# Kernel optimization log

Measured on AMD Instinct MI355X. Metric: run time of the kernel, lower is better.

## Reference

```python
import jax, jax.numpy as jnp
import numpy as np

N_NODES = 50000
N_EDGES = 800000
IN_DIM = 512
HEADS = 4
OUT_DIM = 64


def setup_inputs() -> dict:
    key = jax.random.key(0)
    k1, k2, k3, k4 = jax.random.split(key, 4)
    x = jax.random.normal(k1, (N_NODES, IN_DIM), dtype=jnp.float32)
    edges = jax.random.randint(k2, (N_EDGES, 2), 0, N_NODES, dtype=jnp.int32)
    W = jax.random.normal(k3, (IN_DIM, HEADS * OUT_DIM), dtype=jnp.float32) * 0.05
    a = jax.random.normal(k4, (HEADS, 2 * OUT_DIM), dtype=jnp.float32) * 0.05
    bias = jnp.zeros((HEADS * OUT_DIM,), dtype=jnp.float32)
    return {"x": x, "edges": edges, "W": W, "a": a, "bias": bias}


def reference(x, edges, W, a, bias):
    num_nodes = x.shape[0]
    # project: [N, H, D]
    h = (x @ W).reshape(num_nodes, HEADS, OUT_DIM)
    src = edges[:, 0]
    dst = edges[:, 1]
    # raw attention per edge, per head: e = sum(a * concat(h_src, h_dst))
    a_src = a[:, :OUT_DIM]   # [H, D]
    a_dst = a[:, OUT_DIM:]   # [H, D]
    # precompute per-node dot-products, then gather (avoids [E,H,2D] concat)
    s_src = jnp.einsum('nhd,hd->nh', h, a_src)  # [N, H]
    s_dst = jnp.einsum('nhd,hd->nh', h, a_dst)  # [N, H]
    e = s_src[src] + s_dst[dst]                 # [E, H]
    e = jax.nn.leaky_relu(e, negative_slope=0.2)
    # softmax over edges grouped by SOURCE node (as in original code)
    max_e = jax.ops.segment_max(e, src, num_segments=num_nodes)  # [N, H]
    exp_e = jnp.exp(e - max_e[src])
    sum_exp = jax.ops.segment_sum(exp_e, src, num_segments=num_nodes)
    alpha = exp_e / (sum_exp[src] + 1e-10)       # [E, H]
    # messages aggregated at DESTINATION node
    messages = alpha[:, :, None] * h[src]        # [E, H, D]
    out = jax.ops.segment_sum(messages, dst, num_segments=num_nodes)  # [N, H, D]
    out = out.reshape(num_nodes, HEADS * OUT_DIM) + bias
    return out
```

## Files before the change

### kernel.cpp

```cpp
#include <hip/hip_runtime.h>
#include <math.h>

#define IN_DIM 512
#define NH 4
#define OD 64
#define HD 256

typedef float  floatx4 __attribute__((ext_vector_type(4)));
typedef short  shortx8 __attribute__((ext_vector_type(8)));

__device__ __forceinline__ unsigned short f2bf(float x) {
    unsigned int u = __float_as_uint(x);
    u += 0x7fffu + ((u >> 16) & 1u);
    return (unsigned short)(u >> 16);
}
__device__ __forceinline__ float bf2f(unsigned short u) {
    return __uint_as_float(((unsigned int)u) << 16);
}

__global__ void init_kernel(int* __restrict__ heads, int M2) {
    int i = blockIdx.x * blockDim.x + threadIdx.x;
    if (i < M2) heads[i] = -1;
}

__global__ void convert_w_kernel(const float* __restrict__ W, ushort* __restrict__ Wt) {
    int t = blockIdx.x * blockDim.x + threadIdx.x;
    if (t >= 256 * 64) return;
    int n = t >> 6;
    int k8 = (t & 63) * 8;
    shortx8 v;
    #pragma unroll
    for (int j = 0; j < 8; ++j) v[j] = (short)f2bf(W[(size_t)(k8 + j) * HD + n]);
    *(shortx8*)&Wt[(size_t)n * IN_DIM + k8] = v;
}

__global__ __launch_bounds__(256) void gemm_kernel(const float* __restrict__ x,
                                                   const ushort* __restrict__ Wt,
                                                   ushort* __restrict__ h, int M) {
    __shared__ ushort As[64 * 64];
    __shared__ ushort Bs[256 * 64];
    const int tid = threadIdx.x;
    const int lane = tid & 63;
    const int w = tid >> 6;
    const int bm = blockIdx.x * 64;
    const int wn = w * 64;
    const int lm = lane & 15;
    const int lq = lane >> 4;
    floatx4 acc[4][4];
    #pragma unroll
    for (int i = 0; i < 4; ++i)
        #pragma unroll
        for (int j = 0; j < 4; ++j) acc[i][j] = (floatx4){0.f, 0.f, 0.f, 0.f};

    for (int k0 = 0; k0 < IN_DIM; k0 += 64) {
        #pragma unroll
        for (int j = 0; j < 2; ++j) {
            int ch = tid * 2 + j;
            int row = ch >> 3;
            int c = (ch & 7) ^ (row & 7);
            int gr = bm + row;
            shortx8 v = (shortx8){0, 0, 0, 0, 0, 0, 0, 0};
            if (gr < M) {
                const float* gp = &x[(size_t)gr * IN_DIM + k0 + c * 8];
                float4 v0 = *(const float4*)gp;
                float4 v1 = *(const float4*)(gp + 4);
                v[0] = (short)f2bf(v0.x); v[1] = (short)f2bf(v0.y);
                v[2] = (short)f2bf(v0.z); v[3] = (short)f2bf(v0.w);
                v[4] = (short)f2bf(v1.x); v[5] = (short)f2bf(v1.y);
                v[6] = (short)f2bf(v1.z); v[7] = (short)f2bf(v1.w);
            }
            *(shortx8*)&As[ch * 8] = v;
        }
        #pragma unroll
        for (int j = 0; j < 8; ++j) {
            int ch = j * 256 + tid;
            int row = ch >> 3;
            int c = (ch & 7) ^ (row & 7);
            const ushort* gp = &Wt[(size_t)row * IN_DIM + k0 + c * 8];
            __builtin_amdgcn_global_load_lds(
                (const __attribute__((address_space(1))) void*)gp,
                (__attribute__((address_space(3))) void*)&Bs[(size_t)(j * 256 + wn) * 8],
                16, 0, 0);
        }
        __syncthreads();
        #pragma unroll
        for (int kk = 0; kk < 2; ++kk) {
            shortx8 af[4], bfr[4];
            #pragma unroll
            for (int mt = 0; mt < 4; ++mt) {
                int row = mt * 16 + lm;
                int c = (kk * 4 + lq) ^ (row & 7);
                af[mt] = *(const shortx8*)&As[row * 64 + c * 8];
            }
            #pragma unroll
            for (int nt = 0; nt < 4; ++nt) {
                int row = wn + nt * 16 + lm;
                int c = (kk * 4 + lq) ^ (row & 7);
                bfr[nt] = *(const shortx8*)&Bs[row * 64 + c * 8];
            }
            #pragma unroll
            for (int mt = 0; mt < 4; ++mt)
                #pragma unroll
                for (int nt = 0; nt < 4; ++nt)
                    acc[mt][nt] = __builtin_amdgcn_mfma_f32_16x16x32_bf16(
                        af[mt], bfr[nt], acc[mt][nt], 0, 0, 0);
        }
        __syncthreads();
    }
    #pragma unroll
    for (int mt = 0; mt < 4; ++mt)
        #pragma unroll
        for (int r = 0; r < 4; ++r) {
            int m = bm + mt * 16 + lq * 4 + r;
            if (m < M) {
                #pragma unroll
                for (int nt = 0; nt < 4; ++nt)
                    h[(size_t)m * HD + wn + nt * 16 + lm] = f2bf(acc[mt][nt][r]);
            }
        }
}

__global__ void s_kernel(const ushort* __restrict__ h, const float* __restrict__ a,
                         float* __restrict__ s_src, float* __restrict__ s_dst, int M) {
    int lane = threadIdx.x & 63;
    int n = blockIdx.x * 4 + (threadIdx.x >> 6);
    if (n >= M) return;
    int head = lane >> 4;
    int d0 = (lane & 15) << 2;
    ushort4 hu = *(const ushort4*)&h[(size_t)n * HD + lane * 4];
    float h0 = bf2f(hu.x), h1 = bf2f(hu.y), h2 = bf2f(hu.z), h3 = bf2f(hu.w);
    float4 as = *(const float4*)&a[head * 2 * OD + d0];
    float4 ad = *(const float4*)&a[head * 2 * OD + OD + d0];
    float ps = h0 * as.x + h1 * as.y + h2 * as.z + h3 * as.w;
    float pd = h0 * ad.x + h1 * ad.y + h2 * ad.z + h3 * ad.w;
    #pragma unroll
    for (int off = 1; off < 16; off <<= 1) {
        ps += __shfl_xor(ps, off, 64);
        pd += __shfl_xor(pd, off, 64);
    }
    if ((lane & 15) == 0) {
        s_src[n * NH + head] = ps;
        s_dst[n * NH + head] = pd;
    }
}

__global__ void link_kernel(const int2* __restrict__ edges,
                            int* __restrict__ head_src, int* __restrict__ next_src,
                            int* __restrict__ head_dst, int* __restrict__ next_dst,
                            int E) {
    int i = blockIdx.x * blockDim.x + threadIdx.x;
    if (i >= E) return;
    int2 e = edges[i];
    next_src[i] = atomicExch(&head_src[e.x], i);
    next_dst[i] = atomicExch(&head_dst[e.y], i);
}

__global__ void src_sum_kernel(const int2* __restrict__ edges,
                               const int* __restrict__ head_src,
                               const int* __restrict__ next_src,
                               const float* __restrict__ s_src,
                               const float* __restrict__ s_dst,
                               float* __restrict__ inv_sum, int M) {
    int n = blockIdx.x * blockDim.x + threadIdx.x;
    if (n >= M) return;
    float4 ss = *(const float4*)&s_src[n * NH];
    float4 sum = make_float4(0.f, 0.f, 0.f, 0.f);
    for (int e = head_src[n]; e != -1;) {
        int nxt = next_src[e];
        int dst = edges[e].y;
        float4 sd = *(const float4*)&s_dst[dst * NH];
        float e0 = ss.x + sd.x, e1 = ss.y + sd.y, e2 = ss.z + sd.z, e3 = ss.w + sd.w;
        e0 = e0 > 0.f ? e0 : 0.2f * e0;
        e1 = e1 > 0.f ? e1 : 0.2f * e1;
        e2 = e2 > 0.f ? e2 : 0.2f * e2;
        e3 = e3 > 0.f ? e3 : 0.2f * e3;
        sum.x += __expf(e0); sum.y += __expf(e1);
        sum.z += __expf(e2); sum.w += __expf(e3);
        e = nxt;
    }
    float4 iv;
    iv.x = 1.f / (sum.x + 1e-10f); iv.y = 1.f / (sum.y + 1e-10f);
    iv.z = 1.f / (sum.z + 1e-10f); iv.w = 1.f / (sum.w + 1e-10f);
    *(float4*)&inv_sum[n * NH] = iv;
}

__global__ void gather_kernel(const int2* __restrict__ edges,
                              const int* __restrict__ head_dst,
                              const int* __restrict__ next_dst,
                              const float* __restrict__ s_src,
                              const float* __restrict__ s_dst,
                              const float* __restrict__ inv_sum,
                              const ushort* __restrict__ h,
                              const float* __restrict__ bias,
                              float* __restrict__ out, int M) {
    int lane = threadIdx.x & 63;
    int n = blockIdx.x * 4 + (threadIdx.x >> 6);
    if (n >= M) return;
    int head = lane >> 4;
    float sdst = s_dst[n * NH + head];
    float4 acc = *(const float4*)&bias[lane * 4];
    for (int e = head_dst[n]; e != -1;) {
        int nxt = next_dst[e];
        int src = edges[e].x;
        float es = s_src[src * NH + head] + sdst;
        es = es > 0.f ? es : 0.2f * es;
        float al = __expf(es) * inv_sum[src * NH + head];
        ushort4 hu = *(const ushort4*)&h[(size_t)src * HD + lane * 4];
        acc.x += al * bf2f(hu.x); acc.y += al * bf2f(hu.y);
        acc.z += al * bf2f(hu.z); acc.w += al * bf2f(hu.w);
        e = nxt;
    }
    *(float4*)&out[(size_t)n * HD + lane * 4] = acc;
}

extern "C" void kernel_launch(void* const* d_in, const int* in_sizes, int n_in,
                              void* d_out, int out_size, void* d_ws, size_t ws_size,
                              hipStream_t stream) {
    const float* x     = (const float*)d_in[0];
    const int2*  edges = (const int2*)d_in[1];
    const float* W     = (const float*)d_in[2];
    const float* a     = (const float*)d_in[3];
    const float* bias  = (const float*)d_in[4];
    float* out = (float*)d_out;
    const int M = in_sizes[0] / IN_DIM;
    const int E = in_sizes[1] / 2;

    char* p = (char*)d_ws;
    ushort* hB       = (ushort*)p; p += (size_t)M * HD * sizeof(ushort);
    ushort* Wt       = (ushort*)p; p += (size_t)HD * IN_DIM * sizeof(ushort);
    float*  s_src    = (float*)p;  p += (size_t)M * NH * sizeof(float);
    float*  s_dst    = (float*)p;  p += (size_t)M * NH * sizeof(float);
    float*  inv_sum  = (float*)p;  p += (size_t)M * NH * sizeof(float);
    int*    head_src = (int*)p;    p += (size_t)M * sizeof(int);
    int*    head_dst = (int*)p;    p += (size_t)M * sizeof(int);
    int*    next_src = (int*)p;    p += (size_t)E * sizeof(int);
    int*    next_dst = (int*)p;    p += (size_t)E * sizeof(int);

    init_kernel<<<(2 * M + 255) / 256, 256, 0, stream>>>(head_src, 2 * M);
    convert_w_kernel<<<64, 256, 0, stream>>>(W, Wt);
    gemm_kernel<<<(M + 63) / 64, 256, 0, stream>>>(x, Wt, hB, M);
    s_kernel<<<(M + 3) / 4, 256, 0, stream>>>(hB, a, s_src, s_dst, M);
    link_kernel<<<(E + 255) / 256, 256, 0, stream>>>(edges, head_src, next_src,
                                                     head_dst, next_dst, E);
    src_sum_kernel<<<(M + 255) / 256, 256, 0, stream>>>(edges, head_src, next_src,
                                                        s_src, s_dst, inv_sum, M);
    gather_kernel<<<(M + 3) / 4, 256, 0, stream>>>(edges, head_dst, next_dst,
                                                   s_src, s_dst, inv_sum,
                                                   hB, bias, out, M);
}
```

Before: 406.6 us.

## Fuse attention scores into GEMM epilogue and split edge lists for parallel traversal

Merges init and W conversion into one prep kernel and folds the per-node attention dot products into the GEMM epilogue, which removes the s_kernel launch and its reread of h. Linked lists now carry the neighbour index alongside the next pointer, so the extra edges lookup disappears. Edges are split into two interleaved chains per source and four per destination, giving more independent loads per thread. The gather processes two chains per half-wave with 8-wide bf16 loads and combines the halves with a shuffle. The cost is more atomic head slots, wider next arrays, and a slightly longer GEMM epilogue.

```diff
diff --git a/kernel.cpp b/kernel.cpp
--- a/kernel.cpp
+++ b/kernel.cpp
@@ -18,25 +18,29 @@
     return __uint_as_float(((unsigned int)u) << 16);
 }
 
-__global__ void init_kernel(int* __restrict__ heads, int M2) {
-    int i = blockIdx.x * blockDim.x + threadIdx.x;
-    if (i < M2) heads[i] = -1;
-}
-
-__global__ void convert_w_kernel(const float* __restrict__ W, ushort* __restrict__ Wt) {
+__global__ void prep_kernel(const float* __restrict__ W, ushort* __restrict__ Wt,
+                            int* __restrict__ head_src, int* __restrict__ head_dst,
+                            int M) {
     int t = blockIdx.x * blockDim.x + threadIdx.x;
-    if (t >= 256 * 64) return;
-    int n = t >> 6;
-    int k8 = (t & 63) * 8;
-    shortx8 v;
-    #pragma unroll
-    for (int j = 0; j < 8; ++j) v[j] = (short)f2bf(W[(size_t)(k8 + j) * HD + n]);
-    *(shortx8*)&Wt[(size_t)n * IN_DIM + k8] = v;
+    if (t < 2 * M) head_src[t] = -1;
+    if (t < 4 * M) head_dst[t] = -1;
+    if (t < 256 * 64) {
+        int n = t >> 6;
+        int k8 = (t & 63) * 8;
+        shortx8 v;
+        #pragma unroll
+        for (int j = 0; j < 8; ++j) v[j] = (short)f2bf(W[(size_t)(k8 + j) * HD + n]);
+        *(shortx8*)&Wt[(size_t)n * IN_DIM + k8] = v;
+    }
 }
 
 __global__ __launch_bounds__(256) void gemm_kernel(const float* __restrict__ x,
                                                    const ushort* __restrict__ Wt,
-                                                   ushort* __restrict__ h, int M) {
+                                                   ushort* __restrict__ h,
+                                                   const float* __restrict__ a,
+                                                   float2* __restrict__ ssi,
+                                                   float* __restrict__ s_dst,
+                                                   int M) {
     __shared__ ushort As[64 * 64];
     __shared__ ushort Bs[256 * 64];
     const int tid = threadIdx.x;
@@ -107,6 +111,34 @@
         }
         __syncthreads();
     }
+    float as_l[4], ad_l[4];
+    #pragma unroll
+    for (int nt = 0; nt < 4; ++nt) {
+        as_l[nt] = a[w * 2 * OD + nt * 16 + lm];
+        ad_l[nt] = a[w * 2 * OD + OD + nt * 16 + lm];
+    }
+    #pragma unroll
+    for (int mt = 0; mt < 4; ++mt)
+        #pragma unroll
+        for (int r = 0; r < 4; ++r) {
+            float ps = 0.f, pd = 0.f;
+            #pragma unroll
+            for (int nt = 0; nt < 4; ++nt) {
+                float v = acc[mt][nt][r];
+                ps += v * as_l[nt];
+                pd += v * ad_l[nt];
+            }
+            #pragma unroll
+            for (int off = 1; off < 16; off <<= 1) {
+                ps += __shfl_xor(ps, off, 64);
+                pd += __shfl_xor(pd, off, 64);
+            }
+            int m = bm + mt * 16 + lq * 4 + r;
+            if (m < M && lm == 0) {
+                ssi[m * NH + w].x = ps;
+                s_dst[m * NH + w] = pd;
+            }
+        }
     #pragma unroll
     for (int mt = 0; mt < 4; ++mt)
         #pragma unroll
@@ -120,97 +152,121 @@
         }
 }
 
-__global__ void s_kernel(const ushort* __restrict__ h, const float* __restrict__ a,
-                         float* __restrict__ s_src, float* __restrict__ s_dst, int M) {
-    int lane = threadIdx.x & 63;
-    int n = blockIdx.x * 4 + (threadIdx.x >> 6);
-    if (n >= M) return;
-    int head = lane >> 4;
-    int d0 = (lane & 15) << 2;
-    ushort4 hu = *(const ushort4*)&h[(size_t)n * HD + lane * 4];
-    float h0 = bf2f(hu.x), h1 = bf2f(hu.y), h2 = bf2f(hu.z), h3 = bf2f(hu.w);
-    float4 as = *(const float4*)&a[head * 2 * OD + d0];
-    float4 ad = *(const float4*)&a[head * 2 * OD + OD + d0];
-    float ps = h0 * as.x + h1 * as.y + h2 * as.z + h3 * as.w;
-    float pd = h0 * ad.x + h1 * ad.y + h2 * ad.z + h3 * ad.w;
-    #pragma unroll
-    for (int off = 1; off < 16; off <<= 1) {
-        ps += __shfl_xor(ps, off, 64);
-        pd += __shfl_xor(pd, off, 64);
-    }
-    if ((lane & 15) == 0) {
-        s_src[n * NH + head] = ps;
-        s_dst[n * NH + head] = pd;
-    }
-}
-
 __global__ void link_kernel(const int2* __restrict__ edges,
-                            int* __restrict__ head_src, int* __restrict__ next_src,
-                            int* __restrict__ head_dst, int* __restrict__ next_dst,
+                            int* __restrict__ head_src, int2* __restrict__ next_src,
+                            int* __restrict__ head_dst, int2* __restrict__ next_dst,
                             int E) {
     int i = blockIdx.x * blockDim.x + threadIdx.x;
     if (i >= E) return;
     int2 e = edges[i];
-    next_src[i] = atomicExch(&head_src[e.x], i);
-    next_dst[i] = atomicExch(&head_dst[e.y], i);
-}
-
-__global__ void src_sum_kernel(const int2* __restrict__ edges,
-                               const int* __restrict__ head_src,
-                               const int* __restrict__ next_src,
-                               const float* __restrict__ s_src,
-                               const float* __restrict__ s_dst,
-                               float* __restrict__ inv_sum, int M) {
+    int ps = atomicExch(&head_src[2 * e.x + (i & 1)], i);
+    next_src[i] = make_int2(ps, e.y);
+    int pd = atomicExch(&head_dst[4 * e.y + (i & 3)], i);
+    next_dst[i] = make_int2(pd, e.x);
+}
+
+__global__ void src_sum_kernel(const int* __restrict__ head_src,
+                               const int2* __restrict__ next_src,
+                               float2* __restrict__ ssi,
+                               const float* __restrict__ s_dst, int M) {
     int n = blockIdx.x * blockDim.x + threadIdx.x;
     if (n >= M) return;
-    float4 ss = *(const float4*)&s_src[n * NH];
+    float ss0 = ssi[n * NH + 0].x, ss1 = ssi[n * NH + 1].x;
+    float ss2 = ssi[n * NH + 2].x, ss3 = ssi[n * NH + 3].x;
     float4 sum = make_float4(0.f, 0.f, 0.f, 0.f);
-    for (int e = head_src[n]; e != -1;) {
-        int nxt = next_src[e];
-        int dst = edges[e].y;
-        float4 sd = *(const float4*)&s_dst[dst * NH];
-        float e0 = ss.x + sd.x, e1 = ss.y + sd.y, e2 = ss.z + sd.z, e3 = ss.w + sd.w;
-        e0 = e0 > 0.f ? e0 : 0.2f * e0;
-        e1 = e1 > 0.f ? e1 : 0.2f * e1;
-        e2 = e2 > 0.f ? e2 : 0.2f * e2;
-        e3 = e3 > 0.f ? e3 : 0.2f * e3;
-        sum.x += __expf(e0); sum.y += __expf(e1);
-        sum.z += __expf(e2); sum.w += __expf(e3);
-        e = nxt;
-    }
-    float4 iv;
-    iv.x = 1.f / (sum.x + 1e-10f); iv.y = 1.f / (sum.y + 1e-10f);
-    iv.z = 1.f / (sum.z + 1e-10f); iv.w = 1.f / (sum.w + 1e-10f);
-    *(float4*)&inv_sum[n * NH] = iv;
-}
-
-__global__ void gather_kernel(const int2* __restrict__ edges,
-                              const int* __restrict__ head_dst,
-                              const int* __restrict__ next_dst,
-                              const float* __restrict__ s_src,
+    int e0 = head_src[2 * n], e1 = head_src[2 * n + 1];
+    while (e0 != -1 || e1 != -1) {
+        if (e0 != -1) {
+            int2 t = next_src[e0];
+            float4 sd = *(const float4*)&s_dst[t.y * NH];
+            float a0 = ss0 + sd.x, a1 = ss1 + sd.y, a2 = ss2 + sd.z, a3 = ss3 + sd.w;
+            a0 = a0 > 0.f ? a0 : 0.2f * a0;
+            a1 = a1 > 0.f ? a1 : 0.2f * a1;
+            a2 = a2 > 0.f ? a2 : 0.2f * a2;
+            a3 = a3 > 0.f ? a3 : 0.2f * a3;
+            sum.x += __expf(a0); sum.y += __expf(a1);
+            sum.z += __expf(a2); sum.w += __expf(a3);
+            e0 = t.x;
+        }
+        if (e1 != -1) {
+            int2 t = next_src[e1];
+            float4 sd = *(const float4*)&s_dst[t.y * NH];
+            float a0 = ss0 + sd.x, a1 = ss1 + sd.y, a2 = ss2 + sd.z, a3 = ss3 + sd.w;
+            a0 = a0 > 0.f ? a0 : 0.2f * a0;
+            a1 = a1 > 0.f ? a1 : 0.2f * a1;
+            a2 = a2 > 0.f ? a2 : 0.2f * a2;
+            a3 = a3 > 0.f ? a3 : 0.2f * a3;
+            sum.x += __expf(a0); sum.y += __expf(a1);
+            sum.z += __expf(a2); sum.w += __expf(a3);
+            e1 = t.x;
+        }
+    }
+    ssi[n * NH + 0].y = 1.f / (sum.x + 1e-10f);
+    ssi[n * NH + 1].y = 1.f / (sum.y + 1e-10f);
+    ssi[n * NH + 2].y = 1.f / (sum.z + 1e-10f);
+    ssi[n * NH + 3].y = 1.f / (sum.w + 1e-10f);
+}
+
+__global__ void gather_kernel(const int* __restrict__ head_dst,
+                              const int2* __restrict__ next_dst,
+                              const float2* __restrict__ ssi,
                               const float* __restrict__ s_dst,
-                              const float* __restrict__ inv_sum,
                               const ushort* __restrict__ h,
                               const float* __restrict__ bias,
                               float* __restrict__ out, int M) {
     int lane = threadIdx.x & 63;
     int n = blockIdx.x * 4 + (threadIdx.x >> 6);
     if (n >= M) return;
-    int head = lane >> 4;
+    int half = lane >> 5;
+    int l5 = lane & 31;
+    int head = l5 >> 3;
+    int c0 = l5 * 8;
     float sdst = s_dst[n * NH + head];
-    float4 acc = *(const float4*)&bias[lane * 4];
-    for (int e = head_dst[n]; e != -1;) {
-        int nxt = next_dst[e];
-        int src = edges[e].x;
-        float es = s_src[src * NH + head] + sdst;
-        es = es > 0.f ? es : 0.2f * es;
-        float al = __expf(es) * inv_sum[src * NH + head];
-        ushort4 hu = *(const ushort4*)&h[(size_t)src * HD + lane * 4];
-        acc.x += al * bf2f(hu.x); acc.y += al * bf2f(hu.y);
-        acc.z += al * bf2f(hu.z); acc.w += al * bf2f(hu.w);
-        e = nxt;
-    }
-    *(float4*)&out[(size_t)n * HD + lane * 4] = acc;
+    floatx4 accA = {0.f, 0.f, 0.f, 0.f}, accB = {0.f, 0.f, 0.f, 0.f};
+    int e0 = head_dst[4 * n + 2 * half];
+    int e1 = head_dst[4 * n + 2 * half + 1];
+    while (e0 != -1 || e1 != -1) {
+        if (e0 != -1) {
+            int2 t = next_dst[e0];
+            int src = t.y;
+            float2 si = ssi[src * NH + head];
+            float es = si.x + sdst;
+            es = es > 0.f ? es : 0.2f * es;
+            float al = __expf(es) * si.y;
+            shortx8 hu = *(const shortx8*)&h[(size_t)src * HD + c0];
+            accA.x += al * bf2f((ushort)hu[0]); accA.y += al * bf2f((ushort)hu[1]);
+            accA.z += al * bf2f((ushort)hu[2]); accA.w += al * bf2f((ushort)hu[3]);
+            accB.x += al * bf2f((ushort)hu[4]); accB.y += al * bf2f((ushort)hu[5]);
+            accB.z += al * bf2f((ushort)hu[6]); accB.w += al * bf2f((ushort)hu[7]);
+            e0 = t.x;
+        }
+        if (e1 != -1) {
+            int2 t = next_dst[e1];
+            int src = t.y;
+            float2 si = ssi[src * NH + head];
+            float es = si.x + sdst;
+            es = es > 0.f ? es : 0.2f * es;
+            float al = __expf(es) * si.y;
+            shortx8 hu = *(const shortx8*)&h[(size_t)src * HD + c0];
+            accA.x += al * bf2f((ushort)hu[0]); accA.y += al * bf2f((ushort)hu[1]);
+            accA.z += al * bf2f((ushort)hu[2]); accA.w += al * bf2f((ushort)hu[3]);
+            accB.x += al * bf2f((ushort)hu[4]); accB.y += al * bf2f((ushort)hu[5]);
+            accB.z += al * bf2f((ushort)hu[6]); accB.w += al * bf2f((ushort)hu[7]);
+            e1 = t.x;
+        }
+    }
+    accA.x += __shfl_xor(accA.x, 32, 64); accA.y += __shfl_xor(accA.y, 32, 64);
+    accA.z += __shfl_xor(accA.z, 32, 64); accA.w += __shfl_xor(accA.w, 32, 64);
+    accB.x += __shfl_xor(accB.x, 32, 64); accB.y += __shfl_xor(accB.y, 32, 64);
+    accB.z += __shfl_xor(accB.z, 32, 64); accB.w += __shfl_xor(accB.w, 32, 64);
+    if (half == 0) {
+        float4 b0 = *(const float4*)&bias[c0];
+        float4 b1 = *(const float4*)&bias[c0 + 4];
+        float4 o0 = make_float4(accA.x + b0.x, accA.y + b0.y, accA.z + b0.z, accA.w + b0.w);
+        float4 o1 = make_float4(accB.x + b1.x, accB.y + b1.y, accB.z + b1.z, accB.w + b1.w);
+        *(float4*)&out[(size_t)n * HD + c0] = o0;
+        *(float4*)&out[(size_t)n * HD + c0 + 4] = o1;
+    }
 }
 
 extern "C" void kernel_launch(void* const* d_in, const int* in_sizes, int n_in,
@@ -228,23 +284,18 @@
     char* p = (char*)d_ws;
     ushort* hB       = (ushort*)p; p += (size_t)M * HD * sizeof(ushort);
     ushort* Wt       = (ushort*)p; p += (size_t)HD * IN_DIM * sizeof(ushort);
-    float*  s_src    = (float*)p;  p += (size_t)M * NH * sizeof(float);
     float*  s_dst    = (float*)p;  p += (size_t)M * NH * sizeof(float);
-    float*  inv_sum  = (float*)p;  p += (size_t)M * NH * sizeof(float);
-    int*    head_src = (int*)p;    p += (size_t)M * sizeof(int);
-    int*    head_dst = (int*)p;    p += (size_t)M * sizeof(int);
-    int*    next_src = (int*)p;    p += (size_t)E * sizeof(int);
-    int*    next_dst = (int*)p;    p += (size_t)E * sizeof(int);
-
-    init_kernel<<<(2 * M + 255) / 256, 256, 0, stream>>>(head_src, 2 * M);
-    convert_w_kernel<<<64, 256, 0, stream>>>(W, Wt);
-    gemm_kernel<<<(M + 63) / 64, 256, 0, stream>>>(x, Wt, hB, M);
-    s_kernel<<<(M + 3) / 4, 256, 0, stream>>>(hB, a, s_src, s_dst, M);
+    float2* ssi      = (float2*)p; p += (size_t)M * NH * sizeof(float2);
+    int*    head_src = (int*)p;    p += (size_t)2 * M * sizeof(int);
+    int*    head_dst = (int*)p;    p += (size_t)4 * M * sizeof(int);
+    int2*   next_src = (int2*)p;   p += (size_t)E * sizeof(int2);
+    int2*   next_dst = (int2*)p;   p += (size_t)E * sizeof(int2);
+
+    prep_kernel<<<(4 * M + 255) / 256, 256, 0, stream>>>(W, Wt, head_src, head_dst, M);
+    gemm_kernel<<<(M + 63) / 64, 256, 0, stream>>>(x, Wt, hB, a, ssi, s_dst, M);
     link_kernel<<<(E + 255) / 256, 256, 0, stream>>>(edges, head_src, next_src,
                                                      head_dst, next_dst, E);
-    src_sum_kernel<<<(M + 255) / 256, 256, 0, stream>>>(edges, head_src, next_src,
-                                                        s_src, s_dst, inv_sum, M);
-    gather_kernel<<<(M + 3) / 4, 256, 0, stream>>>(edges, head_dst, next_dst,
-                                                   s_src, s_dst, inv_sum,
+    src_sum_kernel<<<(M + 255) / 256, 256, 0, stream>>>(head_src, next_src, ssi, s_dst, M);
+    gather_kernel<<<(M + 3) / 4, 256, 0, stream>>>(head_dst, next_dst, ssi, s_dst,
                                                    hB, bias, out, M);
 }
```

Result: faster. 367.3 us (-9.7%).
